# Optimization experiments

Hardware: AMD Instinct MI355X
Metric: run time of the kernel (lower is better)

## Reference

```python
import jax, jax.numpy as jnp
import numpy as np

B, IN_C, H, W = 64, 64, 32, 32
OUT_C, KH, KW = 64, 3, 3
STRIDE, PAD, DIL = 1, 1, 1
OUT_H = (H + 2 * PAD - DIL * (KH - 1) - 1) // STRIDE + 1  # 32
OUT_W = (W + 2 * PAD - DIL * (KW - 1) - 1) // STRIDE + 1  # 32


def setup_inputs() -> dict:
    key = jax.random.key(0)
    kx, kw, kb = jax.random.split(key, 3)
    x = jax.random.normal(kx, (B, IN_C, H, W), dtype=jnp.float32)
    n = IN_C * KH * KW
    stdv = 1.0 / np.sqrt(n)
    weight = jax.random.uniform(kw, (OUT_H, OUT_W, OUT_C, IN_C, KH, KW),
                                dtype=jnp.float32, minval=-stdv, maxval=stdv)
    bias = jax.random.uniform(kb, (OUT_C, OUT_H, OUT_W),
                              dtype=jnp.float32, minval=-stdv, maxval=stdv)
    return {"x": x, "weight": weight, "bias": bias}


def _im2col(x):
    # x: [B, C, H, W] -> cols: [B, C*KH*KW, OUT_H*OUT_W], torch.unfold channel-major order
    xp = jnp.pad(x, ((0, 0), (0, 0), (PAD, PAD), (PAD, PAD)))
    patches = []
    for kh in range(KH):
        for kw in range(KW):
            h0, w0 = kh * DIL, kw * DIL
            patches.append(xp[:, :,
                              h0:h0 + (OUT_H - 1) * STRIDE + 1:STRIDE,
                              w0:w0 + (OUT_W - 1) * STRIDE + 1:STRIDE])
    cols = jnp.stack(patches, axis=2)  # [B, C, KH*KW, OUT_H, OUT_W]
    return cols.reshape(x.shape[0], x.shape[1] * KH * KW, OUT_H * OUT_W)


def reference(x, weight, bias):
    cols = _im2col(x)  # [B, K, L] with K = inC*kH*kW, L = outH*outW
    w = weight.reshape(OUT_H * OUT_W, OUT_C, IN_C * KH * KW)  # [L, outC, K]
    # per-location matmul: out[b, l, o] = sum_k cols[b, k, l] * w[l, o, k]
    out = jnp.einsum('bkl,lok->blo', cols, w)
    out = out.reshape(x.shape[0], OUT_H, OUT_W, OUT_C).transpose(0, 3, 1, 2)
    return out + bias[None]
```

## Files before the change

kernel.cpp:

```cpp
#include <hip/hip_runtime.h>
#include <hip/hip_bf16.h>

typedef __attribute__((ext_vector_type(8))) short short8;
typedef __attribute__((ext_vector_type(4))) float f32x4;

__device__ __forceinline__ unsigned short f2bf(float f) {
    union { float f; unsigned int u; } v; v.f = f;
    unsigned int u = v.u;
    u = (u + 0x7FFFu + ((u >> 16) & 1u)) >> 16;
    return (unsigned short)u;
}

__global__ __launch_bounds__(256) void k_xt(const float* __restrict__ x,
                                            unsigned short* __restrict__ xt) {
    const int h  = blockIdx.x;
    const int cg = blockIdx.y;
    const int t  = threadIdx.x;
    __shared__ unsigned short L[32 * 520];

    #pragma unroll
    for (int i = 0; i < 16; ++i) {
        int s   = t + i * 256;
        int row = s >> 3;
        int wq  = s & 7;
        int b = row >> 3, c = row & 7;
        const f32x4 v = *(const f32x4*)(x + (((size_t)(b * 64 + cg * 8 + c) * 32 + h) * 32 + wq * 4));
        int base = c * 64 + b;
        L[(wq * 4 + 0) * 520 + base] = f2bf(v[0]);
        L[(wq * 4 + 1) * 520 + base] = f2bf(v[1]);
        L[(wq * 4 + 2) * 520 + base] = f2bf(v[2]);
        L[(wq * 4 + 3) * 520 + base] = f2bf(v[3]);
    }
    __syncthreads();
    #pragma unroll
    for (int i = 0; i < 8; ++i) {
        int s  = t + i * 256;
        int w  = s >> 6;
        int ch = s & 63;
        short8 v = *(const short8*)&L[w * 520 + ch * 8];
        *(short8*)(xt + (((size_t)(h * 32 + w) * 64 + cg * 8) * 64 + ch * 8)) = v;
    }
}

__global__ __launch_bounds__(256) void k_main(const float* __restrict__ wgt,
                                              const unsigned short* __restrict__ xt,
                                              const float* __restrict__ bias,
                                              unsigned short* __restrict__ ws2b) {
    const int bid = blockIdx.x;
    const int l   = (bid & 7) * 128 + (bid >> 3);
    const int oh = l >> 5, ow = l & 31;
    const int t  = threadIdx.x;
    const int wave = t >> 6, lane = t & 63;
    const int wm = wave >> 1, wn = wave & 1;

    __shared__ unsigned short Ash[2][64 * 72];
    __shared__ unsigned short Bsh[2][64 * 72];

    f32x4 acc[2][2];
    #pragma unroll
    for (int i = 0; i < 2; ++i)
        #pragma unroll
        for (int j = 0; j < 2; ++j)
            acc[i][j] = (f32x4){0.f, 0.f, 0.f, 0.f};

    const float* wslab = wgt + (size_t)l * (64 * 576);
    const int b0 = wave * 16;
    const int o  = t >> 2, kp = t & 3;
    const float* bbase = wslab + o * 576 + kp * 16;

    auto loadA = [&](int kt, short8& va, short8& vb) {
        int kk = kt * 64 + lane;
        int c  = kk / 9;
        int r  = kk - c * 9;
        int kh = r / 3;
        int kw = r - kh * 3;
        int hh = oh + kh - 1;
        int ww = ow + kw - 1;
        va = (short8){0,0,0,0,0,0,0,0};
        vb = (short8){0,0,0,0,0,0,0,0};
        if ((unsigned)hh < 32u && (unsigned)ww < 32u) {
            const unsigned short* src = xt + (((size_t)(hh * 32 + ww) * 64 + c) * 64 + b0);
            va = *(const short8*)src;
            vb = *(const short8*)(src + 8);
        }
    };
    auto loadB = [&](int kt, f32x4& w0, f32x4& w1, f32x4& w2, f32x4& w3) {
        const f32x4* bp = (const f32x4*)(bbase + kt * 64);
        w0 = bp[0]; w1 = bp[1]; w2 = bp[2]; w3 = bp[3];
    };

    short8 cA0, cA1;
    short8 nA0 = (short8){0,0,0,0,0,0,0,0}, nA1 = (short8){0,0,0,0,0,0,0,0};
    f32x4 cB0, cB1, cB2, cB3;
    f32x4 nB0 = (f32x4){0,0,0,0}, nB1 = nB0, nB2 = nB0, nB3 = nB0;

    loadA(0, cA0, cA1);
    loadB(0, cB0, cB1, cB2, cB3);

    for (int kt = 0; kt < 9; ++kt) {
        const int p = kt & 1;
        if (kt < 8) {
            loadA(kt + 1, nA0, nA1);
            loadB(kt + 1, nB0, nB1, nB2, nB3);
        }
        #pragma unroll
        for (int j = 0; j < 8; ++j) Ash[p][(b0 + j) * 72 + lane] = (unsigned short)cA0[j];
        #pragma unroll
        for (int j = 0; j < 8; ++j) Ash[p][(b0 + 8 + j) * 72 + lane] = (unsigned short)cA1[j];
        {
            short8 p0, p1;
            p0[0] = (short)f2bf(cB0[0]); p0[1] = (short)f2bf(cB0[1]);
            p0[2] = (short)f2bf(cB0[2]); p0[3] = (short)f2bf(cB0[3]);
            p0[4] = (short)f2bf(cB1[0]); p0[5] = (short)f2bf(cB1[1]);
            p0[6] = (short)f2bf(cB1[2]); p0[7] = (short)f2bf(cB1[3]);
            p1[0] = (short)f2bf(cB2[0]); p1[1] = (short)f2bf(cB2[1]);
            p1[2] = (short)f2bf(cB2[2]); p1[3] = (short)f2bf(cB2[3]);
            p1[4] = (short)f2bf(cB3[0]); p1[5] = (short)f2bf(cB3[1]);
            p1[6] = (short)f2bf(cB3[2]); p1[7] = (short)f2bf(cB3[3]);
            unsigned short* bdst = &Bsh[p][o * 72 + kp * 16];
            *(short8*)bdst       = p0;
            *(short8*)(bdst + 8) = p1;
        }
        asm volatile("s_waitcnt lgkmcnt(0)" ::: "memory");
        __builtin_amdgcn_s_barrier();
        __builtin_amdgcn_sched_barrier(0);
        #pragma unroll
        for (int ks = 0; ks < 2; ++ks) {
            int kof = ks * 32 + (lane >> 4) * 8;
            short8 a0 = *(const short8*)&Ash[p][(wm * 32 + (lane & 15)) * 72 + kof];
            short8 a1 = *(const short8*)&Ash[p][(wm * 32 + 16 + (lane & 15)) * 72 + kof];
            short8 q0 = *(const short8*)&Bsh[p][(wn * 32 + (lane & 15)) * 72 + kof];
            short8 q1 = *(const short8*)&Bsh[p][(wn * 32 + 16 + (lane & 15)) * 72 + kof];
            acc[0][0] = __builtin_amdgcn_mfma_f32_16x16x32_bf16(a0, q0, acc[0][0], 0, 0, 0);
            acc[0][1] = __builtin_amdgcn_mfma_f32_16x16x32_bf16(a0, q1, acc[0][1], 0, 0, 0);
            acc[1][0] = __builtin_amdgcn_mfma_f32_16x16x32_bf16(a1, q0, acc[1][0], 0, 0, 0);
            acc[1][1] = __builtin_amdgcn_mfma_f32_16x16x32_bf16(a1, q1, acc[1][1], 0, 0, 0);
        }
        cA0 = nA0; cA1 = nA1;
        cB0 = nB0; cB1 = nB1; cB2 = nB2; cB3 = nB3;
    }

    const int col = lane & 15;
    const int rq  = (lane >> 4) * 4;
    #pragma unroll
    for (int j = 0; j < 2; ++j) {
        int n = wn * 32 + j * 16 + col;
        float bv = bias[n * 1024 + l];
        #pragma unroll
        for (int i = 0; i < 2; ++i) {
            int mbase = wm * 32 + i * 16 + rq;
            #pragma unroll
            for (int q = 0; q < 4; ++q) {
                ws2b[(size_t)l * 4096 + (size_t)(mbase + q) * 64 + n] = f2bf(acc[i][j][q] + bv);
            }
        }
    }
}

__global__ __launch_bounds__(256) void k_out(const unsigned short* __restrict__ ws2b,
                                             float* __restrict__ out) {
    const int bx = blockIdx.x;
    const int lt = bx & 15;
    const int mt = bx >> 4;
    const int t  = threadIdx.x;
    __shared__ float T[64 * 65];
    const int l0 = lt * 64, m0 = mt * 64;

    #pragma unroll
    for (int i = 0; i < 2; ++i) {
        int s  = t + i * 256;
        int lr = s >> 3;
        int mc = (s & 7) * 8;
        short8 v = *(const short8*)&ws2b[(size_t)(l0 + lr) * 4096 + m0 + mc];
        #pragma unroll
        for (int j = 0; j < 8; ++j) {
            union { unsigned int u; float f; } w;
            w.u = ((unsigned int)(unsigned short)v[j]) << 16;
            T[lr * 65 + mc + j] = w.f;
        }
    }
    __syncthreads();
    #pragma unroll
    for (int i = 0; i < 4; ++i) {
        int s  = t + i * 256;
        int mr = s >> 4;
        int lc = (s & 15) * 4;
        f32x4 v;
        v[0] = T[(lc + 0) * 65 + mr];
        v[1] = T[(lc + 1) * 65 + mr];
        v[2] = T[(lc + 2) * 65 + mr];
        v[3] = T[(lc + 3) * 65 + mr];
        *(f32x4*)(out + (size_t)(m0 + mr) * 1024 + l0 + lc) = v;
    }
}

__global__ __launch_bounds__(256) void k_naive(const float* __restrict__ x,
                                               const float* __restrict__ wgt,
                                               const float* __restrict__ bias,
                                               float* __restrict__ out) {
    int idx = blockIdx.x * 256 + threadIdx.x;
    int ow = idx & 31, oh = (idx >> 5) & 31, o = (idx >> 10) & 63, b = idx >> 16;
    float acc = bias[(o * 32 + oh) * 32 + ow];
    const float* wp = wgt + ((size_t)(oh * 32 + ow) * 64 + o) * 576;
    for (int c = 0; c < 64; ++c) {
        for (int kh = 0; kh < 3; ++kh) {
            int hh = oh + kh - 1;
            if ((unsigned)hh >= 32u) continue;
            for (int kw = 0; kw < 3; ++kw) {
                int ww = ow + kw - 1;
                if ((unsigned)ww >= 32u) continue;
                acc += x[((size_t)(b * 64 + c) * 32 + hh) * 32 + ww] * wp[c * 9 + kh * 3 + kw];
            }
        }
    }
    out[idx] = acc;
}

extern "C" void kernel_launch(void* const* d_in, const int* in_sizes, int n_in,
                              void* d_out, int out_size, void* d_ws, size_t ws_size,
                              hipStream_t stream) {
    const float* x    = (const float*)d_in[0];
    const float* wgt  = (const float*)d_in[1];
    const float* bias = (const float*)d_in[2];
    float* out = (float*)d_out;

    const size_t xt_bytes  = (size_t)32 * 32 * 64 * 64 * 2;
    const size_t ws2_bytes = (size_t)1024 * 4096 * 2;

    if (ws_size >= xt_bytes + ws2_bytes) {
        unsigned short* xt   = (unsigned short*)d_ws;
        unsigned short* ws2b = (unsigned short*)((char*)d_ws + xt_bytes);
        k_xt<<<dim3(32, 8), 256, 0, stream>>>(x, xt);
        k_main<<<1024, 256, 0, stream>>>(wgt, xt, bias, ws2b);
        k_out<<<1024, 256, 0, stream>>>(ws2b, out);
    } else {
        k_naive<<<(64 * 64 * 32 * 32) / 256, 256, 0, stream>>>(x, wgt, bias, out);
    }
}
```

Before: 46.12 us.

## Fuse output transpose into main GEMM kernel, two locations per block

Merges the per-location GEMM and the output-transpose kernel into one kernel. Each block now handles two adjacent output locations, staging results in shared memory and writing float2 pairs straight to the NCHW output. This removes the bf16 intermediate workspace round-trip and one launch, and drops the extra bf16 rounding of the output. The cost is half as many blocks (512) and 8-byte strided output stores, which are less coalesced than the previous 16-byte transposed writes.

```diff
diff --git a/kernel.cpp b/kernel.cpp
--- a/kernel.cpp
+++ b/kernel.cpp
@@ -3,6 +3,7 @@
 
 typedef __attribute__((ext_vector_type(8))) short short8;
 typedef __attribute__((ext_vector_type(4))) float f32x4;
+typedef __attribute__((ext_vector_type(2))) float f32x2;
 
 __device__ __forceinline__ unsigned short f2bf(float f) {
     union { float f; unsigned int u; } v; v.f = f;
@@ -42,40 +43,42 @@
     }
 }
 
-__global__ __launch_bounds__(256) void k_main(const float* __restrict__ wgt,
-                                              const unsigned short* __restrict__ xt,
-                                              const float* __restrict__ bias,
-                                              unsigned short* __restrict__ ws2b) {
-    const int bid = blockIdx.x;
-    const int l   = (bid & 7) * 128 + (bid >> 3);
-    const int oh = l >> 5, ow = l & 31;
-    const int t  = threadIdx.x;
+__global__ __launch_bounds__(256) void k_fused(const float* __restrict__ wgt,
+                                               const unsigned short* __restrict__ xt,
+                                               const float* __restrict__ bias,
+                                               float* __restrict__ out) {
+    const int bid  = blockIdx.x;
+    const int tile = (bid & 7) * 64 + (bid >> 3);
+    const int l0   = tile * 2;
+    const int oh   = l0 >> 5;
+    const int ow0  = l0 & 31;
+    const int t    = threadIdx.x;
     const int wave = t >> 6, lane = t & 63;
     const int wm = wave >> 1, wn = wave & 1;
 
-    __shared__ unsigned short Ash[2][64 * 72];
-    __shared__ unsigned short Bsh[2][64 * 72];
-
-    f32x4 acc[2][2];
-    #pragma unroll
-    for (int i = 0; i < 2; ++i)
+    __shared__ unsigned short S[4][64 * 72];
+
+    f32x4 acc[2][2][2];
+    #pragma unroll
+    for (int li = 0; li < 2; ++li)
         #pragma unroll
-        for (int j = 0; j < 2; ++j)
-            acc[i][j] = (f32x4){0.f, 0.f, 0.f, 0.f};
-
-    const float* wslab = wgt + (size_t)l * (64 * 576);
+        for (int i = 0; i < 2; ++i)
+            #pragma unroll
+            for (int j = 0; j < 2; ++j)
+                acc[li][i][j] = (f32x4){0.f, 0.f, 0.f, 0.f};
+
     const int b0 = wave * 16;
     const int o  = t >> 2, kp = t & 3;
-    const float* bbase = wslab + o * 576 + kp * 16;
-
-    auto loadA = [&](int kt, short8& va, short8& vb) {
+    const float* bbase = wgt + (size_t)l0 * (64 * 576) + o * 576 + kp * 16;
+
+    auto loadA = [&](int li, int kt, short8& va, short8& vb) {
         int kk = kt * 64 + lane;
         int c  = kk / 9;
         int r  = kk - c * 9;
         int kh = r / 3;
         int kw = r - kh * 3;
         int hh = oh + kh - 1;
-        int ww = ow + kw - 1;
+        int ww = ow0 + li + kw - 1;
         va = (short8){0,0,0,0,0,0,0,0};
         vb = (short8){0,0,0,0,0,0,0,0};
         if ((unsigned)hh < 32u && (unsigned)ww < 32u) {
@@ -84,113 +87,93 @@
             vb = *(const short8*)(src + 8);
         }
     };
-    auto loadB = [&](int kt, f32x4& w0, f32x4& w1, f32x4& w2, f32x4& w3) {
-        const f32x4* bp = (const f32x4*)(bbase + kt * 64);
+    auto loadB = [&](int li, int kt, f32x4& w0, f32x4& w1, f32x4& w2, f32x4& w3) {
+        const f32x4* bp = (const f32x4*)(bbase + (size_t)li * 36864 + kt * 64);
         w0 = bp[0]; w1 = bp[1]; w2 = bp[2]; w3 = bp[3];
     };
 
     short8 cA0, cA1;
-    short8 nA0 = (short8){0,0,0,0,0,0,0,0}, nA1 = (short8){0,0,0,0,0,0,0,0};
+    short8 nA0 = (short8){0,0,0,0,0,0,0,0}, nA1 = nA0;
     f32x4 cB0, cB1, cB2, cB3;
     f32x4 nB0 = (f32x4){0,0,0,0}, nB1 = nB0, nB2 = nB0, nB3 = nB0;
 
-    loadA(0, cA0, cA1);
-    loadB(0, cB0, cB1, cB2, cB3);
-
-    for (int kt = 0; kt < 9; ++kt) {
-        const int p = kt & 1;
-        if (kt < 8) {
-            loadA(kt + 1, nA0, nA1);
-            loadB(kt + 1, nB0, nB1, nB2, nB3);
-        }
-        #pragma unroll
-        for (int j = 0; j < 8; ++j) Ash[p][(b0 + j) * 72 + lane] = (unsigned short)cA0[j];
-        #pragma unroll
-        for (int j = 0; j < 8; ++j) Ash[p][(b0 + 8 + j) * 72 + lane] = (unsigned short)cA1[j];
-        {
-            short8 p0, p1;
-            p0[0] = (short)f2bf(cB0[0]); p0[1] = (short)f2bf(cB0[1]);
-            p0[2] = (short)f2bf(cB0[2]); p0[3] = (short)f2bf(cB0[3]);
-            p0[4] = (short)f2bf(cB1[0]); p0[5] = (short)f2bf(cB1[1]);
-            p0[6] = (short)f2bf(cB1[2]); p0[7] = (short)f2bf(cB1[3]);
-            p1[0] = (short)f2bf(cB2[0]); p1[1] = (short)f2bf(cB2[1]);
-            p1[2] = (short)f2bf(cB2[2]); p1[3] = (short)f2bf(cB2[3]);
-            p1[4] = (short)f2bf(cB3[0]); p1[5] = (short)f2bf(cB3[1]);
-            p1[6] = (short)f2bf(cB3[2]); p1[7] = (short)f2bf(cB3[3]);
-            unsigned short* bdst = &Bsh[p][o * 72 + kp * 16];
-            *(short8*)bdst       = p0;
-            *(short8*)(bdst + 8) = p1;
-        }
-        asm volatile("s_waitcnt lgkmcnt(0)" ::: "memory");
-        __builtin_amdgcn_s_barrier();
-        __builtin_amdgcn_sched_barrier(0);
-        #pragma unroll
-        for (int ks = 0; ks < 2; ++ks) {
-            int kof = ks * 32 + (lane >> 4) * 8;
-            short8 a0 = *(const short8*)&Ash[p][(wm * 32 + (lane & 15)) * 72 + kof];
-            short8 a1 = *(const short8*)&Ash[p][(wm * 32 + 16 + (lane & 15)) * 72 + kof];
-            short8 q0 = *(const short8*)&Bsh[p][(wn * 32 + (lane & 15)) * 72 + kof];
-            short8 q1 = *(const short8*)&Bsh[p][(wn * 32 + 16 + (lane & 15)) * 72 + kof];
-            acc[0][0] = __builtin_amdgcn_mfma_f32_16x16x32_bf16(a0, q0, acc[0][0], 0, 0, 0);
-            acc[0][1] = __builtin_amdgcn_mfma_f32_16x16x32_bf16(a0, q1, acc[0][1], 0, 0, 0);
-            acc[1][0] = __builtin_amdgcn_mfma_f32_16x16x32_bf16(a1, q0, acc[1][0], 0, 0, 0);
-            acc[1][1] = __builtin_amdgcn_mfma_f32_16x16x32_bf16(a1, q1, acc[1][1], 0, 0, 0);
-        }
-        cA0 = nA0; cA1 = nA1;
-        cB0 = nB0; cB1 = nB1; cB2 = nB2; cB3 = nB3;
-    }
-
+    loadA(0, 0, cA0, cA1);
+    loadB(0, 0, cB0, cB1, cB2, cB3);
+
+    #pragma unroll
+    for (int li = 0; li < 2; ++li) {
+        for (int kt = 0; kt < 9; ++kt) {
+            const int p = (li + kt) & 1;
+            if (!(li == 1 && kt == 8)) {
+                int lin = (kt == 8) ? li + 1 : li;
+                int ktn = (kt == 8) ? 0 : kt + 1;
+                loadA(lin, ktn, nA0, nA1);
+                loadB(lin, ktn, nB0, nB1, nB2, nB3);
+            }
+            #pragma unroll
+            for (int j = 0; j < 8; ++j) S[p][(b0 + j) * 72 + lane] = (unsigned short)cA0[j];
+            #pragma unroll
+            for (int j = 0; j < 8; ++j) S[p][(b0 + 8 + j) * 72 + lane] = (unsigned short)cA1[j];
+            {
+                short8 p0, p1;
+                p0[0] = (short)f2bf(cB0[0]); p0[1] = (short)f2bf(cB0[1]);
+                p0[2] = (short)f2bf(cB0[2]); p0[3] = (short)f2bf(cB0[3]);
+                p0[4] = (short)f2bf(cB1[0]); p0[5] = (short)f2bf(cB1[1]);
+                p0[6] = (short)f2bf(cB1[2]); p0[7] = (short)f2bf(cB1[3]);
+                p1[0] = (short)f2bf(cB2[0]); p1[1] = (short)f2bf(cB2[1]);
+                p1[2] = (short)f2bf(cB2[2]); p1[3] = (short)f2bf(cB2[3]);
+                p1[4] = (short)f2bf(cB3[0]); p1[5] = (short)f2bf(cB3[1]);
+                p1[6] = (short)f2bf(cB3[2]); p1[7] = (short)f2bf(cB3[3]);
+                unsigned short* bdst = &S[2 + p][o * 72 + kp * 16];
+                *(short8*)bdst       = p0;
+                *(short8*)(bdst + 8) = p1;
+            }
+            asm volatile("s_waitcnt lgkmcnt(0)" ::: "memory");
+            __builtin_amdgcn_s_barrier();
+            __builtin_amdgcn_sched_barrier(0);
+            #pragma unroll
+            for (int ks = 0; ks < 2; ++ks) {
+                int kof = ks * 32 + (lane >> 4) * 8;
+                short8 a0 = *(const short8*)&S[p][(wm * 32 + (lane & 15)) * 72 + kof];
+                short8 a1 = *(const short8*)&S[p][(wm * 32 + 16 + (lane & 15)) * 72 + kof];
+                short8 q0 = *(const short8*)&S[2 + p][(wn * 32 + (lane & 15)) * 72 + kof];
+                short8 q1 = *(const short8*)&S[2 + p][(wn * 32 + 16 + (lane & 15)) * 72 + kof];
+                acc[li][0][0] = __builtin_amdgcn_mfma_f32_16x16x32_bf16(a0, q0, acc[li][0][0], 0, 0, 0);
+                acc[li][0][1] = __builtin_amdgcn_mfma_f32_16x16x32_bf16(a0, q1, acc[li][0][1], 0, 0, 0);
+                acc[li][1][0] = __builtin_amdgcn_mfma_f32_16x16x32_bf16(a1, q0, acc[li][1][0], 0, 0, 0);
+                acc[li][1][1] = __builtin_amdgcn_mfma_f32_16x16x32_bf16(a1, q1, acc[li][1][1], 0, 0, 0);
+            }
+            cA0 = nA0; cA1 = nA1;
+            cB0 = nB0; cB1 = nB1; cB2 = nB2; cB3 = nB3;
+        }
+    }
+
+    __syncthreads();
+    float* F = (float*)S;
     const int col = lane & 15;
     const int rq  = (lane >> 4) * 4;
     #pragma unroll
     for (int j = 0; j < 2; ++j) {
         int n = wn * 32 + j * 16 + col;
-        float bv = bias[n * 1024 + l];
         #pragma unroll
-        for (int i = 0; i < 2; ++i) {
-            int mbase = wm * 32 + i * 16 + rq;
-            #pragma unroll
-            for (int q = 0; q < 4; ++q) {
-                ws2b[(size_t)l * 4096 + (size_t)(mbase + q) * 64 + n] = f2bf(acc[i][j][q] + bv);
-            }
-        }
-    }
-}
-
-__global__ __launch_bounds__(256) void k_out(const unsigned short* __restrict__ ws2b,
-                                             float* __restrict__ out) {
-    const int bx = blockIdx.x;
-    const int lt = bx & 15;
-    const int mt = bx >> 4;
-    const int t  = threadIdx.x;
-    __shared__ float T[64 * 65];
-    const int l0 = lt * 64, m0 = mt * 64;
-
-    #pragma unroll
-    for (int i = 0; i < 2; ++i) {
-        int s  = t + i * 256;
-        int lr = s >> 3;
-        int mc = (s & 7) * 8;
-        short8 v = *(const short8*)&ws2b[(size_t)(l0 + lr) * 4096 + m0 + mc];
-        #pragma unroll
-        for (int j = 0; j < 8; ++j) {
-            union { unsigned int u; float f; } w;
-            w.u = ((unsigned int)(unsigned short)v[j]) << 16;
-            T[lr * 65 + mc + j] = w.f;
+        for (int li = 0; li < 2; ++li) {
+            float bv = bias[n * 1024 + l0 + li];
+            #pragma unroll
+            for (int i = 0; i < 2; ++i) {
+                int mbase = wm * 32 + i * 16 + rq;
+                #pragma unroll
+                for (int q = 0; q < 4; ++q) {
+                    F[((mbase + q) * 64 + n) * 2 + li] = acc[li][i][j][q] + bv;
+                }
+            }
         }
     }
     __syncthreads();
     #pragma unroll
-    for (int i = 0; i < 4; ++i) {
-        int s  = t + i * 256;
-        int mr = s >> 4;
-        int lc = (s & 15) * 4;
-        f32x4 v;
-        v[0] = T[(lc + 0) * 65 + mr];
-        v[1] = T[(lc + 1) * 65 + mr];
-        v[2] = T[(lc + 2) * 65 + mr];
-        v[3] = T[(lc + 3) * 65 + mr];
-        *(f32x4*)(out + (size_t)(m0 + mr) * 1024 + l0 + lc) = v;
+    for (int i = 0; i < 16; ++i) {
+        int r = t + i * 256;
+        f32x2 v = *(const f32x2*)&F[r * 2];
+        *(f32x2*)(out + (size_t)r * 1024 + l0) = v;
     }
 }
 
@@ -224,15 +207,12 @@
     const float* bias = (const float*)d_in[2];
     float* out = (float*)d_out;
 
-    const size_t xt_bytes  = (size_t)32 * 32 * 64 * 64 * 2;
-    const size_t ws2_bytes = (size_t)1024 * 4096 * 2;
-
-    if (ws_size >= xt_bytes + ws2_bytes) {
-        unsigned short* xt   = (unsigned short*)d_ws;
-        unsigned short* ws2b = (unsigned short*)((char*)d_ws + xt_bytes);
+    const size_t xt_bytes = (size_t)32 * 32 * 64 * 64 * 2;
+
+    if (ws_size >= xt_bytes) {
+        unsigned short* xt = (unsigned short*)d_ws;
         k_xt<<<dim3(32, 8), 256, 0, stream>>>(x, xt);
-        k_main<<<1024, 256, 0, stream>>>(wgt, xt, bias, ws2b);
-        k_out<<<1024, 256, 0, stream>>>(ws2b, out);
+        k_fused<<<512, 256, 0, stream>>>(wgt, xt, bias, out);
     } else {
         k_naive<<<(64 * 64 * 32 * 32) / 256, 256, 0, stream>>>(x, wgt, bias, out);
     }
```

Result: slower. 49.27 us (+6.8%).

## Load weight fragments directly into MFMA registers, bypassing shared memory

Applied to the files above, without the earlier changes.

The B operand (per-location weights) is now read from global memory straight into the register layout the MFMA expects, with no staging through shared memory. This removes the Bsh buffer, its LDS writes and reads, and part of the barrier traffic. Conversion to bf16 now uses the packed __float22bfloat162_rn intrinsic, and launch bounds ask for 4 blocks per CU. The cost is that weights are read redundantly: wm=0 and wm=1 waves load the same B rows, doubling weight global/L2 traffic, and the extra register pressure may constrain occupancy.

```diff
diff --git a/kernel.cpp b/kernel.cpp
--- a/kernel.cpp
+++ b/kernel.cpp
@@ -9,6 +9,15 @@
     unsigned int u = v.u;
     u = (u + 0x7FFFu + ((u >> 16) & 1u)) >> 16;
     return (unsigned short)u;
+}
+
+__device__ __forceinline__ short8 cvt8(const f32x4 a, const f32x4 b) {
+    union { __hip_bfloat162 h[4]; short8 s; } r;
+    r.h[0] = __float22bfloat162_rn(make_float2(a[0], a[1]));
+    r.h[1] = __float22bfloat162_rn(make_float2(a[2], a[3]));
+    r.h[2] = __float22bfloat162_rn(make_float2(b[0], b[1]));
+    r.h[3] = __float22bfloat162_rn(make_float2(b[2], b[3]));
+    return r.s;
 }
 
 __global__ __launch_bounds__(256) void k_xt(const float* __restrict__ x,
@@ -42,10 +51,10 @@
     }
 }
 
-__global__ __launch_bounds__(256) void k_main(const float* __restrict__ wgt,
-                                              const unsigned short* __restrict__ xt,
-                                              const float* __restrict__ bias,
-                                              unsigned short* __restrict__ ws2b) {
+__global__ __launch_bounds__(256, 4) void k_main(const float* __restrict__ wgt,
+                                                 const unsigned short* __restrict__ xt,
+                                                 const float* __restrict__ bias,
+                                                 unsigned short* __restrict__ ws2b) {
     const int bid = blockIdx.x;
     const int l   = (bid & 7) * 128 + (bid >> 3);
     const int oh = l >> 5, ow = l & 31;
@@ -54,7 +63,6 @@
     const int wm = wave >> 1, wn = wave & 1;
 
     __shared__ unsigned short Ash[2][64 * 72];
-    __shared__ unsigned short Bsh[2][64 * 72];
 
     f32x4 acc[2][2];
     #pragma unroll
@@ -63,10 +71,11 @@
         for (int j = 0; j < 2; ++j)
             acc[i][j] = (f32x4){0.f, 0.f, 0.f, 0.f};
 
-    const float* wslab = wgt + (size_t)l * (64 * 576);
     const int b0 = wave * 16;
-    const int o  = t >> 2, kp = t & 3;
-    const float* bbase = wslab + o * 576 + kp * 16;
+
+    const int klane = (lane >> 4) * 8;
+    const float* brow0 = wgt + (size_t)l * 36864 + (size_t)(wn * 32 + (lane & 15)) * 576 + klane;
+    const float* brow1 = brow0 + 16 * 576;
 
     auto loadA = [&](int kt, short8& va, short8& vb) {
         int kk = kt * 64 + lane;
@@ -84,60 +93,53 @@
             vb = *(const short8*)(src + 8);
         }
     };
-    auto loadB = [&](int kt, f32x4& w0, f32x4& w1, f32x4& w2, f32x4& w3) {
-        const f32x4* bp = (const f32x4*)(bbase + kt * 64);
-        w0 = bp[0]; w1 = bp[1]; w2 = bp[2]; w3 = bp[3];
+    auto loadB = [&](int kt, f32x4 (&bf)[4][2]) {
+        #pragma unroll
+        for (int f = 0; f < 4; ++f) {
+            const float* q = ((f & 1) ? brow1 : brow0) + kt * 64 + (f >> 1) * 32;
+            bf[f][0] = *(const f32x4*)q;
+            bf[f][1] = *(const f32x4*)(q + 4);
+        }
     };
 
     short8 cA0, cA1;
-    short8 nA0 = (short8){0,0,0,0,0,0,0,0}, nA1 = (short8){0,0,0,0,0,0,0,0};
-    f32x4 cB0, cB1, cB2, cB3;
-    f32x4 nB0 = (f32x4){0,0,0,0}, nB1 = nB0, nB2 = nB0, nB3 = nB0;
+    short8 nA0 = (short8){0,0,0,0,0,0,0,0}, nA1 = nA0;
+    f32x4 bf[4][2];
+    short8 bq[4];
 
     loadA(0, cA0, cA1);
-    loadB(0, cB0, cB1, cB2, cB3);
+    loadB(0, bf);
+    #pragma unroll
+    for (int f = 0; f < 4; ++f) bq[f] = cvt8(bf[f][0], bf[f][1]);
 
     for (int kt = 0; kt < 9; ++kt) {
         const int p = kt & 1;
         if (kt < 8) {
             loadA(kt + 1, nA0, nA1);
-            loadB(kt + 1, nB0, nB1, nB2, nB3);
+            loadB(kt + 1, bf);
         }
         #pragma unroll
         for (int j = 0; j < 8; ++j) Ash[p][(b0 + j) * 72 + lane] = (unsigned short)cA0[j];
         #pragma unroll
         for (int j = 0; j < 8; ++j) Ash[p][(b0 + 8 + j) * 72 + lane] = (unsigned short)cA1[j];
-        {
-            short8 p0, p1;
-            p0[0] = (short)f2bf(cB0[0]); p0[1] = (short)f2bf(cB0[1]);
-            p0[2] = (short)f2bf(cB0[2]); p0[3] = (short)f2bf(cB0[3]);
-            p0[4] = (short)f2bf(cB1[0]); p0[5] = (short)f2bf(cB1[1]);
-            p0[6] = (short)f2bf(cB1[2]); p0[7] = (short)f2bf(cB1[3]);
-            p1[0] = (short)f2bf(cB2[0]); p1[1] = (short)f2bf(cB2[1]);
-            p1[2] = (short)f2bf(cB2[2]); p1[3] = (short)f2bf(cB2[3]);
-            p1[4] = (short)f2bf(cB3[0]); p1[5] = (short)f2bf(cB3[1]);
-            p1[6] = (short)f2bf(cB3[2]); p1[7] = (short)f2bf(cB3[3]);
-            unsigned short* bdst = &Bsh[p][o * 72 + kp * 16];
-            *(short8*)bdst       = p0;
-            *(short8*)(bdst + 8) = p1;
-        }
         asm volatile("s_waitcnt lgkmcnt(0)" ::: "memory");
         __builtin_amdgcn_s_barrier();
         __builtin_amdgcn_sched_barrier(0);
         #pragma unroll
         for (int ks = 0; ks < 2; ++ks) {
-            int kof = ks * 32 + (lane >> 4) * 8;
+            int kof = ks * 32 + klane;
             short8 a0 = *(const short8*)&Ash[p][(wm * 32 + (lane & 15)) * 72 + kof];
             short8 a1 = *(const short8*)&Ash[p][(wm * 32 + 16 + (lane & 15)) * 72 + kof];
-            short8 q0 = *(const short8*)&Bsh[p][(wn * 32 + (lane & 15)) * 72 + kof];
-            short8 q1 = *(const short8*)&Bsh[p][(wn * 32 + 16 + (lane & 15)) * 72 + kof];
-            acc[0][0] = __builtin_amdgcn_mfma_f32_16x16x32_bf16(a0, q0, acc[0][0], 0, 0, 0);
-            acc[0][1] = __builtin_amdgcn_mfma_f32_16x16x32_bf16(a0, q1, acc[0][1], 0, 0, 0);
-            acc[1][0] = __builtin_amdgcn_mfma_f32_16x16x32_bf16(a1, q0, acc[1][0], 0, 0, 0);
-            acc[1][1] = __builtin_amdgcn_mfma_f32_16x16x32_bf16(a1, q1, acc[1][1], 0, 0, 0);
+            acc[0][0] = __builtin_amdgcn_mfma_f32_16x16x32_bf16(a0, bq[ks * 2 + 0], acc[0][0], 0, 0, 0);
+            acc[0][1] = __builtin_amdgcn_mfma_f32_16x16x32_bf16(a0, bq[ks * 2 + 1], acc[0][1], 0, 0, 0);
+            acc[1][0] = __builtin_amdgcn_mfma_f32_16x16x32_bf16(a1, bq[ks * 2 + 0], acc[1][0], 0, 0, 0);
+            acc[1][1] = __builtin_amdgcn_mfma_f32_16x16x32_bf16(a1, bq[ks * 2 + 1], acc[1][1], 0, 0, 0);
         }
         cA0 = nA0; cA1 = nA1;
-        cB0 = nB0; cB1 = nB1; cB2 = nB2; cB3 = nB3;
+        if (kt < 8) {
+            #pragma unroll
+            for (int f = 0; f < 4; ++f) bq[f] = cvt8(bf[f][0], bf[f][1]);
+        }
     }
 
     const int col = lane & 15;
```

New measurement: 60.87 us. +32.0%, slower.
